# Kernel tuning notes

Hardware: AMD Instinct MI355X
Metric: run time of the kernel (lower is better)

Reference implementation:

```python
import jax, jax.numpy as jnp
import numpy as np

B, H, L, E, M = 16, 8, 4096, 64, 64


def setup_inputs() -> dict:
    key = jax.random.key(0)
    k1, k2, k3 = jax.random.split(key, 3)
    x = jax.random.normal(k1, (B, H, L, E), dtype=jnp.float32)
    # nn.Parameter(torch.randn(E, E, M, 2) / sqrt(E))
    weights = jax.random.normal(k2, (E, E, M, 2), dtype=jnp.float32) / np.float32(np.sqrt(E))
    # torch.randperm(L//2)[:M].sort()[0] -> sorted unique mode indices in [0, L//2)
    index = jnp.sort(jax.random.permutation(k3, L // 2)[:M]).astype(jnp.int32)
    return {"x": x, "weights": weights, "index": index}


def reference(x, weights, index):
    Bx, Hx, Lx, Ex = x.shape
    xt = jnp.swapaxes(x, -1, -2)                      # [B,H,E,L]
    x_ft = jnp.fft.rfft(xt, axis=-1)                  # [B,H,E,L//2+1] complex64
    w_c = jax.lax.complex(weights[..., 0], weights[..., 1])  # [E,E,M] complex
    sel = x_ft[..., index]                            # gather K modes: [B,H,E,M]
    out_sel = jnp.einsum('bhei,eoi->bhoi', sel, w_c)  # per-mode complex matmul
    out_ft = jnp.zeros_like(x_ft).at[..., index].set(out_sel)  # scatter back
    out = jnp.fft.irfft(out_ft, n=Lx, axis=-1)        # [B,H,E,L] real
    return jnp.swapaxes(out, -1, -2)                  # [B,H,L,E]
```

## Files before the change

### kernel.cpp

```cpp
#include <hip/hip_runtime.h>

using half8 = __attribute__((ext_vector_type(8))) _Float16;
using f32x4 = __attribute__((ext_vector_type(4))) float;

#define Lc 4096
#define Ec 64
#define Mc 64
#define BHc 128

#define TWO_PI_OVER_L 1.5339807878856412e-3f

__global__ __launch_bounds__(256) void twid_k(const int* __restrict__ idx,
                                              _Float16* __restrict__ Tt,
                                              _Float16* __restrict__ UL) {
    int id = blockIdx.x * 256 + threadIdx.x;
    {
        int l = id >> 7, m2 = id & 127, m = m2 & 63;
        int k = idx[m];
        int ph = (k * l) & (Lc - 1);
        float s, c;
        sincosf((float)ph * TWO_PI_OVER_L, &s, &c);
        UL[id] = (_Float16)((m2 >= 64) ? s : c);
    }
    {
        int m2 = id >> 12, l = id & 4095, m = m2 & 63;
        int k = idx[m];
        int ph = (k * l) & (Lc - 1);
        float s, c;
        sincosf((float)ph * TWO_PI_OVER_L, &s, &c);
        Tt[id] = (_Float16)((m2 >= 64) ? -s : c);
    }
}

#define LOADT(SET, S) do{                                                     \
    const float* g0_ = xp + (size_t)((S) * 64 + 2 * lp) * Ec;                 \
    const float* g1_ = xp + (size_t)((S) * 64 + 2 * lp + 32) * Ec;            \
    ra[SET][0] = *(const float4*)g0_;  rb[SET][0] = *(const float4*)(g0_ + Ec);\
    ra[SET][1] = *(const float4*)g1_;  rb[SET][1] = *(const float4*)(g1_ + Ec);\
}while(0)

#define PACKT(SET, BUF) do{                                                   \
    _Pragma("unroll")                                                         \
    for (int i_ = 0; i_ < 2; ++i_) {                                          \
        const float* pa_ = (const float*)&ra[SET][i_];                        \
        const float* pb_ = (const float*)&rb[SET][i_];                        \
        unsigned int pk_[4];                                                  \
        _Pragma("unroll")                                                     \
        for (int j_ = 0; j_ < 4; ++j_) {                                      \
            unsigned short ua_ = __builtin_bit_cast(unsigned short, (_Float16)pa_[j_]); \
            unsigned short ub_ = __builtin_bit_cast(unsigned short, (_Float16)pb_[j_]); \
            pk_[j_] = ua_ | ((unsigned int)ub_ << 16);                        \
        }                                                                     \
        _Pragma("unroll")                                                     \
        for (int j_ = 0; j_ < 4; ++j_) {                                      \
            int jr_ = (j_ + col4) & 3;                                        \
            int e_  = col4 * 4 + jr_;                                         \
            int byt_ = (e_ * 128 + lp * 4 + i_ * 64) ^ ((e_ & 7) << 4);       \
            *(unsigned int*)((char*)xs[BUF] + byt_) = pk_[jr_];               \
        }                                                                     \
    }                                                                         \
}while(0)

#define MFMA_STEP(S, BUF) do{                                                 \
    _Pragma("unroll")                                                         \
    for (int ks_ = 0; ks_ < 2; ++ks_) {                                       \
        half8 A0_ = *(const half8*)(tp + (S) * 64 + ks_ * 32);                \
        half8 A1_ = *(const half8*)(tp + (size_t)16 * Lc + (S) * 64 + ks_ * 32); \
        _Pragma("unroll")                                                     \
        for (int j_ = 0; j_ < 4; ++j_) {                                      \
            int rbyt_ = ((16 * j_ + lo16) * 128 + ks_ * 64 + kg * 16) ^ ((lo16 & 7) << 4); \
            half8 Bv_ = *(const half8*)((const char*)xs[BUF] + rbyt_);        \
            acc[0][j_] = __builtin_amdgcn_mfma_f32_16x16x32_f16(A0_, Bv_, acc[0][j_], 0, 0, 0); \
            acc[1][j_] = __builtin_amdgcn_mfma_f32_16x16x32_f16(A1_, Bv_, acc[1][j_], 0, 0, 0); \
        }                                                                     \
    }                                                                         \
}while(0)

template<int NCH>
__global__ __launch_bounds__(256) void fwd_k(const float* __restrict__ x,
                                             const _Float16* __restrict__ Tt,
                                             float* __restrict__ selP) {
    constexpr int CH = Lc / NCH;
    constexpr int NT = CH / 64;
    __shared__ _Float16 xs[2][64 * 64];
    int bh = blockIdx.x, ch = blockIdx.y;
    int tid = threadIdx.x;
    int lane = tid & 63, w = tid >> 6;
    int lo16 = lane & 15, kg = lane >> 4;
    int col4 = tid & 15, lp = tid >> 4;

    const float* xp = x + ((size_t)bh * Lc + (size_t)ch * CH) * Ec + col4 * 4;
    const _Float16* tp = Tt + (size_t)(w * 32 + lo16) * Lc + ch * CH + kg * 8;

    float4 ra[2][2], rb[2][2];
    LOADT(0, 0);
    LOADT(1, 1);
    PACKT(0, 0);
    __syncthreads();

    f32x4 acc[2][4] = {};
    for (int t = 0; t < NT / 2; ++t) {
        int s0 = 2 * t, s1 = 2 * t + 1;
        if (s0 + 2 < NT) LOADT(0, s0 + 2);
        PACKT(1, 1);
        MFMA_STEP(s0, 0);
        __syncthreads();
        if (s1 + 2 < NT) LOADT(1, s1 + 2);
        if (s1 + 1 < NT) PACKT(0, 0);
        MFMA_STEP(s1, 1);
        __syncthreads();
    }

    float* op = selP + (size_t)(ch * BHc + bh) * (128 * Ec);
    #pragma unroll
    for (int a = 0; a < 2; ++a)
        #pragma unroll
        for (int j = 0; j < 4; ++j)
            #pragma unroll
            for (int r = 0; r < 4; ++r) {
                int m2 = w * 32 + a * 16 + kg * 4 + r;
                int e  = 16 * j + lo16;
                op[m2 * Ec + e] = acc[a][j][r];
            }
}

__global__ __launch_bounds__(256) void mix_k(const float* __restrict__ selP,
                                             const float* __restrict__ wgt,
                                             const int* __restrict__ idx,
                                             _Float16* __restrict__ Vt, int nch) {
    __shared__ float sel_s[64 * 65];
    int bh = blockIdx.x, oh = blockIdx.y, mh = blockIdx.z;
    int tid = threadIdx.x;
    #pragma unroll
    for (int i = 0; i < 4; ++i) {
        int f4 = i * 256 + tid;
        int lr = f4 >> 4, e4 = (f4 & 15) * 4;
        int m2 = (lr < 32) ? (mh * 32 + lr) : (64 + mh * 32 + (lr - 32));
        float4 a = make_float4(0.f, 0.f, 0.f, 0.f);
        for (int chn = 0; chn < nch; ++chn) {
            float4 v = *(const float4*)(selP + (size_t)(chn * BHc + bh) * 8192
                                             + (size_t)m2 * Ec + e4);
            a.x += v.x; a.y += v.y; a.z += v.z; a.w += v.w;
        }
        float* dst = &sel_s[lr * 65 + e4];
        dst[0] = a.x; dst[1] = a.y; dst[2] = a.z; dst[3] = a.w;
    }
    __syncthreads();
    int og = tid & 15, mg = tid >> 4;
    int o0 = oh * 32 + og * 2;
    int m0 = mh * 32 + mg * 2;
    int lm = mg * 2;
    float rR[2][2] = {{0}}, rI[2][2] = {{0}};
    #pragma unroll 8
    for (int e = 0; e < Ec; ++e) {
        float sr0 = sel_s[lm * 65 + e];
        float sr1 = sel_s[(lm + 1) * 65 + e];
        float si0 = sel_s[(32 + lm) * 65 + e];
        float si1 = sel_s[(32 + lm + 1) * 65 + e];
        #pragma unroll
        for (int i = 0; i < 2; ++i) {
            const float4* wp = (const float4*)&wgt[(((size_t)e * Ec + (o0 + i)) * Mc + m0) * 2];
            float4 wv = *wp;
            rR[i][0] += sr0 * wv.x - si0 * wv.y;
            rI[i][0] += sr0 * wv.y + si0 * wv.x;
            rR[i][1] += sr1 * wv.z - si1 * wv.w;
            rI[i][1] += sr1 * wv.w + si1 * wv.z;
        }
    }
    float s0 = (idx[m0] == 0 ? 1.0f : 2.0f) / (float)Lc;
    float s1 = (idx[m0 + 1] == 0 ? 1.0f : 2.0f) / (float)Lc;
    #pragma unroll
    for (int i = 0; i < 2; ++i) {
        _Float16* vp = Vt + ((size_t)bh * 64 + o0 + i) * 128;
        unsigned short r0 = __builtin_bit_cast(unsigned short, (_Float16)(rR[i][0] * s0));
        unsigned short r1 = __builtin_bit_cast(unsigned short, (_Float16)(rR[i][1] * s1));
        unsigned short i0 = __builtin_bit_cast(unsigned short, (_Float16)(-rI[i][0] * s0));
        unsigned short i1 = __builtin_bit_cast(unsigned short, (_Float16)(-rI[i][1] * s1));
        *(unsigned int*)&vp[m0]      = r0 | ((unsigned int)r1 << 16);
        *(unsigned int*)&vp[64 + m0] = i0 | ((unsigned int)i1 << 16);
    }
}

__global__ __launch_bounds__(256) void inv_k(const _Float16* __restrict__ UL,
                                             const _Float16* __restrict__ Vt,
                                             float* __restrict__ out) {
    __shared__ _Float16 vs[64 * 136];
    int bh = blockIdx.x, lb = blockIdx.y;
    int tid = threadIdx.x, lane = tid & 63, w = tid >> 6;
    int lo16 = lane & 15, kg = lane >> 4;
    #pragma unroll
    for (int i = 0; i < 4; ++i) {
        int f = i * 256 + tid;
        int row = f >> 4, seg = f & 15;
        uint4 t4 = *(const uint4*)(Vt + (size_t)bh * 8192 + row * 128 + seg * 8);
        *(uint4*)&vs[row * 136 + seg * 8] = t4;
    }
    __syncthreads();
    int lt0 = lb * 256 + w * 64;
    const _Float16* up = UL + (size_t)(lt0 + lo16) * 128 + kg * 8;
    f32x4 acc[4][4] = {};
    #pragma unroll
    for (int ks = 0; ks < 4; ++ks) {
        half8 Af[4];
        #pragma unroll
        for (int a = 0; a < 4; ++a)
            Af[a] = *(const half8*)(up + (size_t)a * 16 * 128 + ks * 32);
        #pragma unroll
        for (int j = 0; j < 4; ++j) {
            half8 Bf = *(const half8*)&vs[(16 * j + lo16) * 136 + ks * 32 + kg * 8];
            #pragma unroll
            for (int a = 0; a < 4; ++a)
                acc[a][j] = __builtin_amdgcn_mfma_f32_16x16x32_f16(Af[a], Bf, acc[a][j], 0, 0, 0);
        }
    }
    float* op = out + ((size_t)bh * Lc + lt0) * Ec;
    #pragma unroll
    for (int a = 0; a < 4; ++a)
        #pragma unroll
        for (int j = 0; j < 4; ++j)
            #pragma unroll
            for (int r = 0; r < 4; ++r) {
                int ll = a * 16 + kg * 4 + r;
                int o  = 16 * j + lo16;
                op[ll * Ec + o] = acc[a][j][r];
            }
}

extern "C" void kernel_launch(void* const* d_in, const int* in_sizes, int n_in,
                              void* d_out, int out_size, void* d_ws, size_t ws_size,
                              hipStream_t stream) {
    const float* x   = (const float*)d_in[0];
    const float* wgt = (const float*)d_in[1];
    const int*   idx = (const int*)d_in[2];
    float* out = (float*)d_out;

    size_t need8 = (size_t)8 * BHc * 8192 * 4 + (2ull * 128 * Lc + (size_t)BHc * 8192) * 2;
    int nch = (ws_size >= need8) ? 8 : 4;

    char* ws = (char*)d_ws;
    float*    selP = (float*)ws;
    _Float16* Tt   = (_Float16*)(ws + (size_t)nch * BHc * 8192 * 4);
    _Float16* UL   = Tt + (size_t)128 * Lc;
    _Float16* Vt   = UL + (size_t)Lc * 128;

    twid_k<<<2048, 256, 0, stream>>>(idx, Tt, UL);
    if (nch == 8)
        fwd_k<8><<<dim3(BHc, 8), 256, 0, stream>>>(x, Tt, selP);
    else
        fwd_k<4><<<dim3(BHc, 4), 256, 0, stream>>>(x, Tt, selP);
    mix_k<<<dim3(BHc, 2, 2), 256, 0, stream>>>(selP, wgt, idx, Vt, nch);
    inv_k<<<dim3(BHc, 16), 256, 0, stream>>>(UL, Vt, out);
}
```

Before: 123.0 us.

## Use fast sin/cos intrinsics, remap mix_k threads, stage inv_k output through LDS

The twiddle kernel now computes its angles with __sinf/__cosf instead of sincosf. mix_k is regridded to 4 m-quarters per bh, with each thread owning one output channel and four modes, so weight loads become two consecutive float4 per e. inv_k writes its MFMA accumulators to a per-wave LDS scratch and then stores full float4 rows, replacing scattered scalar global stores with coalesced vector writes. The extra LDS round trip and __syncthreads add some overhead, and the fast intrinsics are slightly less accurate.

```diff
diff --git a/kernel.cpp b/kernel.cpp
--- a/kernel.cpp
+++ b/kernel.cpp
@@ -18,17 +18,15 @@
         int l = id >> 7, m2 = id & 127, m = m2 & 63;
         int k = idx[m];
         int ph = (k * l) & (Lc - 1);
-        float s, c;
-        sincosf((float)ph * TWO_PI_OVER_L, &s, &c);
-        UL[id] = (_Float16)((m2 >= 64) ? s : c);
+        float ang = (float)ph * TWO_PI_OVER_L;
+        UL[id] = (_Float16)((m2 >= 64) ? __sinf(ang) : __cosf(ang));
     }
     {
         int m2 = id >> 12, l = id & 4095, m = m2 & 63;
         int k = idx[m];
         int ph = (k * l) & (Lc - 1);
-        float s, c;
-        sincosf((float)ph * TWO_PI_OVER_L, &s, &c);
-        Tt[id] = (_Float16)((m2 >= 64) ? -s : c);
+        float ang = (float)ph * TWO_PI_OVER_L;
+        Tt[id] = (_Float16)((m2 >= 64) ? -__sinf(ang) : __cosf(ang));
     }
 }
 
@@ -128,14 +126,14 @@
                                              const float* __restrict__ wgt,
                                              const int* __restrict__ idx,
                                              _Float16* __restrict__ Vt, int nch) {
-    __shared__ float sel_s[64 * 65];
-    int bh = blockIdx.x, oh = blockIdx.y, mh = blockIdx.z;
+    __shared__ float sel_s[32 * 65];
+    int bh = blockIdx.x, mh = blockIdx.y;
     int tid = threadIdx.x;
     #pragma unroll
-    for (int i = 0; i < 4; ++i) {
+    for (int i = 0; i < 2; ++i) {
         int f4 = i * 256 + tid;
         int lr = f4 >> 4, e4 = (f4 & 15) * 4;
-        int m2 = (lr < 32) ? (mh * 32 + lr) : (64 + mh * 32 + (lr - 32));
+        int m2 = (lr < 16) ? (mh * 16 + lr) : (64 + mh * 16 + (lr - 16));
         float4 a = make_float4(0.f, 0.f, 0.f, 0.f);
         for (int chn = 0; chn < nch; ++chn) {
             float4 v = *(const float4*)(selP + (size_t)(chn * BHc + bh) * 8192
@@ -146,45 +144,42 @@
         dst[0] = a.x; dst[1] = a.y; dst[2] = a.z; dst[3] = a.w;
     }
     __syncthreads();
-    int og = tid & 15, mg = tid >> 4;
-    int o0 = oh * 32 + og * 2;
-    int m0 = mh * 32 + mg * 2;
-    int lm = mg * 2;
-    float rR[2][2] = {{0}}, rI[2][2] = {{0}};
-    #pragma unroll 8
+    int o = tid & 63, mg = tid >> 6;
+    int mloc = mg * 4;
+    int m0 = mh * 16 + mloc;
+    float rR[4] = {0}, rI[4] = {0};
+    #pragma unroll 4
     for (int e = 0; e < Ec; ++e) {
-        float sr0 = sel_s[lm * 65 + e];
-        float sr1 = sel_s[(lm + 1) * 65 + e];
-        float si0 = sel_s[(32 + lm) * 65 + e];
-        float si1 = sel_s[(32 + lm + 1) * 65 + e];
-        #pragma unroll
-        for (int i = 0; i < 2; ++i) {
-            const float4* wp = (const float4*)&wgt[(((size_t)e * Ec + (o0 + i)) * Mc + m0) * 2];
-            float4 wv = *wp;
-            rR[i][0] += sr0 * wv.x - si0 * wv.y;
-            rI[i][0] += sr0 * wv.y + si0 * wv.x;
-            rR[i][1] += sr1 * wv.z - si1 * wv.w;
-            rI[i][1] += sr1 * wv.w + si1 * wv.z;
-        }
-    }
-    float s0 = (idx[m0] == 0 ? 1.0f : 2.0f) / (float)Lc;
-    float s1 = (idx[m0 + 1] == 0 ? 1.0f : 2.0f) / (float)Lc;
-    #pragma unroll
-    for (int i = 0; i < 2; ++i) {
-        _Float16* vp = Vt + ((size_t)bh * 64 + o0 + i) * 128;
-        unsigned short r0 = __builtin_bit_cast(unsigned short, (_Float16)(rR[i][0] * s0));
-        unsigned short r1 = __builtin_bit_cast(unsigned short, (_Float16)(rR[i][1] * s1));
-        unsigned short i0 = __builtin_bit_cast(unsigned short, (_Float16)(-rI[i][0] * s0));
-        unsigned short i1 = __builtin_bit_cast(unsigned short, (_Float16)(-rI[i][1] * s1));
-        *(unsigned int*)&vp[m0]      = r0 | ((unsigned int)r1 << 16);
-        *(unsigned int*)&vp[64 + m0] = i0 | ((unsigned int)i1 << 16);
+        const float4* wp = (const float4*)&wgt[(((size_t)e * Ec + o) * Mc + m0) * 2];
+        float4 w0 = wp[0], w1 = wp[1];
+        float sr0 = sel_s[(mloc + 0) * 65 + e], si0 = sel_s[(16 + mloc + 0) * 65 + e];
+        float sr1 = sel_s[(mloc + 1) * 65 + e], si1 = sel_s[(16 + mloc + 1) * 65 + e];
+        float sr2 = sel_s[(mloc + 2) * 65 + e], si2 = sel_s[(16 + mloc + 2) * 65 + e];
+        float sr3 = sel_s[(mloc + 3) * 65 + e], si3 = sel_s[(16 + mloc + 3) * 65 + e];
+        rR[0] += sr0 * w0.x - si0 * w0.y;  rI[0] += sr0 * w0.y + si0 * w0.x;
+        rR[1] += sr1 * w0.z - si1 * w0.w;  rI[1] += sr1 * w0.w + si1 * w0.z;
+        rR[2] += sr2 * w1.x - si2 * w1.y;  rI[2] += sr2 * w1.y + si2 * w1.x;
+        rR[3] += sr3 * w1.z - si3 * w1.w;  rI[3] += sr3 * w1.w + si3 * w1.z;
+    }
+    _Float16* vp = Vt + ((size_t)bh * 64 + o) * 128;
+    #pragma unroll
+    for (int p = 0; p < 2; ++p) {
+        float s0 = (idx[m0 + 2 * p] == 0 ? 1.0f : 2.0f) / (float)Lc;
+        float s1 = (idx[m0 + 2 * p + 1] == 0 ? 1.0f : 2.0f) / (float)Lc;
+        unsigned short r0 = __builtin_bit_cast(unsigned short, (_Float16)(rR[2 * p] * s0));
+        unsigned short r1 = __builtin_bit_cast(unsigned short, (_Float16)(rR[2 * p + 1] * s1));
+        unsigned short i0 = __builtin_bit_cast(unsigned short, (_Float16)(-rI[2 * p] * s0));
+        unsigned short i1 = __builtin_bit_cast(unsigned short, (_Float16)(-rI[2 * p + 1] * s1));
+        *(unsigned int*)&vp[m0 + 2 * p]      = r0 | ((unsigned int)r1 << 16);
+        *(unsigned int*)&vp[64 + m0 + 2 * p] = i0 | ((unsigned int)i1 << 16);
     }
 }
 
 __global__ __launch_bounds__(256) void inv_k(const _Float16* __restrict__ UL,
                                              const _Float16* __restrict__ Vt,
                                              float* __restrict__ out) {
-    __shared__ _Float16 vs[64 * 136];
+    __shared__ __align__(16) char smem[4 * 1152 * 4];
+    _Float16* vs = (_Float16*)smem;
     int bh = blockIdx.x, lb = blockIdx.y;
     int tid = threadIdx.x, lane = tid & 63, w = tid >> 6;
     int lo16 = lane & 15, kg = lane >> 4;
@@ -213,17 +208,24 @@
                 acc[a][j] = __builtin_amdgcn_mfma_f32_16x16x32_f16(Af[a], Bf, acc[a][j], 0, 0, 0);
         }
     }
+    __syncthreads();
+    float* scr = (float*)smem + w * 1152;
     float* op = out + ((size_t)bh * Lc + lt0) * Ec;
-    #pragma unroll
-    for (int a = 0; a < 4; ++a)
+    int rr = lane >> 4, cc = lane & 15;
+    #pragma unroll
+    for (int a = 0; a < 4; ++a) {
         #pragma unroll
         for (int j = 0; j < 4; ++j)
             #pragma unroll
-            for (int r = 0; r < 4; ++r) {
-                int ll = a * 16 + kg * 4 + r;
-                int o  = 16 * j + lo16;
-                op[ll * Ec + o] = acc[a][j][r];
-            }
+            for (int r = 0; r < 4; ++r)
+                scr[(kg * 4 + r) * 72 + 16 * j + lo16] = acc[a][j][r];
+        #pragma unroll
+        for (int g = 0; g < 4; ++g) {
+            int row = g * 4 + rr;
+            float4 v = *(float4*)&scr[row * 72 + cc * 4];
+            *(float4*)(op + (size_t)(a * 16 + row) * Ec + cc * 4) = v;
+        }
+    }
 }
 
 extern "C" void kernel_launch(void* const* d_in, const int* in_sizes, int n_in,
@@ -248,6 +250,6 @@
         fwd_k<8><<<dim3(BHc, 8), 256, 0, stream>>>(x, Tt, selP);
     else
         fwd_k<4><<<dim3(BHc, 4), 256, 0, stream>>>(x, Tt, selP);
-    mix_k<<<dim3(BHc, 2, 2), 256, 0, stream>>>(selP, wgt, idx, Vt, nch);
+    mix_k<<<dim3(BHc, 4), 256, 0, stream>>>(selP, wgt, idx, Vt, nch);
     inv_k<<<dim3(BHc, 16), 256, 0, stream>>>(UL, Vt, out);
 }
```

New measurement: 130.7 us. 1.06x slower.
